# Optimization experiments

Hardware: AMD Instinct MI355X
Metric: run time of the kernel (lower is better)

Reference implementation:

```python
import jax, jax.numpy as jnp
import numpy as np

H = 4      # num_heads
DH = 32    # head dim (hidden_size // num_heads)


def _seg_softmax(logits, seg, n):
    # numerically stable segment softmax over axis 0, segments of size n
    m = jax.ops.segment_max(logits, seg, num_segments=n)
    e = jnp.exp(logits - m[seg])
    s = jax.ops.segment_sum(e, seg, num_segments=n)
    return e / (s[seg] + 1e-16)


def setup_inputs() -> dict:
    key = jax.random.key(0)
    ks = jax.random.split(key, 16)
    N, E, EE, C = 50000, 400000, 800000, 800000
    NIN, EIN, HID, EMB = 1, 32, 128, 32
    inp = {
        'x': jax.random.normal(ks[0], (N, NIN), jnp.float32),
        'edge_index': jax.random.randint(ks[1], (2, E), 0, N),
        'edge_attr': jax.random.normal(ks[2], (E, EIN), jnp.float32),
        'edge_to_edge_index': jax.random.randint(ks[3], (2, EE), 0, E),
        'node_to_node_index': jax.random.randint(ks[4], (2, C), 0, N),
        'W1': jax.random.normal(ks[5], (2 * NIN + EIN, EMB), jnp.float32) / np.sqrt(2 * NIN + EIN),
        'b1': jnp.zeros((EMB,), jnp.float32),
        'W2': jax.random.normal(ks[6], (EMB, HID), jnp.float32) / np.sqrt(EMB),
        'b2': jnp.zeros((HID,), jnp.float32),
        'Wq': jax.random.normal(ks[7], (HID, HID), jnp.float32) / np.sqrt(HID),
        'Wk': jax.random.normal(ks[8], (HID, HID), jnp.float32) / np.sqrt(HID),
        'Wv': jax.random.normal(ks[9], (HID, HID), jnp.float32) / np.sqrt(HID),
        'Wq2': jax.random.normal(ks[10], (1, HID), jnp.float32),
        'Wk2': jax.random.normal(ks[11], (1, HID), jnp.float32),
        'Wv2': jax.random.normal(ks[12], (1, HID), jnp.float32),
    }
    return inp


def reference(x, edge_index, edge_attr, edge_to_edge_index, node_to_node_index,
              W1, b1, W2, b2, Wq, Wk, Wv, Wq2, Wk2, Wv2):
    N = x.shape[0]
    E = edge_attr.shape[0]
    # --- NodeToEdgeAggregation: gather endpoint node feats, concat edge attr, MLP ---
    s, d = edge_index[0], edge_index[1]
    h = jnp.concatenate([x[s], x[d], edge_attr], axis=-1)          # [E, 2*nin+ein]
    h = jax.nn.relu(h @ W1 + b1) @ W2 + b2                          # [E, hidden]
    # --- EdgeToEdgeAggregation: multi-head attention on the line graph ---
    es, ed = edge_to_edge_index[0], edge_to_edge_index[1]
    q = (h @ Wq)[ed].reshape(-1, H, DH)                             # [EE, H, DH]
    k = (h @ Wk)[es].reshape(-1, H, DH)
    v = (h @ Wv)[es].reshape(-1, H, DH)
    logits = (q * k).sum(-1) / jnp.sqrt(jnp.float32(DH))            # [EE, H]
    alpha = _seg_softmax(logits, ed, E)                             # softmax over incoming edge-neighbors
    agg_e = jax.ops.segment_sum(alpha[..., None] * v, ed, num_segments=E)  # [E, H, DH]
    updated_edge_feat = agg_e.reshape(E, -1).mean(axis=1, keepdims=True)   # [E, 1]
    # --- EdgeToNodeAggregation over combined node+edge feature array ---
    nef = jnp.concatenate([x, updated_edge_feat], axis=0)           # [N+E, 1]
    ns, nd = node_to_node_index[0], node_to_node_index[1]
    q2 = (nef[nd] @ Wq2).reshape(-1, H, DH)                         # [C, H, DH]
    k2 = (nef[ns] @ Wk2).reshape(-1, H, DH)
    v2 = (nef[ns] @ Wv2).reshape(-1, H, DH)
    logits2 = (q2 * k2).sum(-1) / jnp.sqrt(jnp.float32(DH))         # [C, H]
    alpha2 = _seg_softmax(logits2, nd, N + E)
    msgs = (alpha2[..., None] * v2).reshape(ns.shape[0], -1).mean(axis=1)  # [C]
    aggregated_node_feat = jax.ops.segment_sum(msgs, nd, num_segments=N)   # [N]
    return (aggregated_node_feat, updated_edge_feat)
```

## Files before the change

kernel.cpp:

```cpp
#include <hip/hip_runtime.h>
#include <stdint.h>

#define HIDN 128
#define EMBN 32
#define PCAP 16
#define NCAP 64
#define PSEGSH 9
#define NSEGSH 7
#define PSEG (1 << PSEGSH)
#define NSEG (1 << NSEGSH)
#define PBCAP 1408
#define NBCAP 2816
#define CHUNK 2048
#define MAXBINS 800

typedef __attribute__((ext_vector_type(8))) short bf16x8;
typedef __attribute__((ext_vector_type(4))) float f32x4;
typedef unsigned long long u64;

__device__ __forceinline__ unsigned bf16r(float f) {
  unsigned u = __float_as_uint(f);
  return (u + 0x7FFFu + ((u >> 16) & 1u)) >> 16;
}
__device__ __forceinline__ unsigned pack2(float a, float b) {
  return bf16r(a) | (bf16r(b) << 16);
}
__device__ __forceinline__ float blo(unsigned u) { return __uint_as_float(u << 16); }
__device__ __forceinline__ float bhi(unsigned u) { return __uint_as_float(u & 0xFFFF0000u); }
__device__ __forceinline__ float4 f4fma(float s, float4 a, float4 b) {
  return make_float4(fmaf(s, a.x, b.x), fmaf(s, a.y, b.y), fmaf(s, a.z, b.z), fmaf(s, a.w, b.w));
}
__device__ __forceinline__ float4 f4max0(float4 a) {
  return make_float4(fmaxf(a.x, 0.f), fmaxf(a.y, 0.f), fmaxf(a.z, 0.f), fmaxf(a.w, 0.f));
}

__global__ __launch_bounds__(256) void k_prep1(
    const float* __restrict__ W2, const float* __restrict__ b2,
    const float* __restrict__ Wq, const float* __restrict__ Wk, const float* __restrict__ Wv,
    float* __restrict__ Wqp, float* __restrict__ Wkp, float* __restrict__ bqp,
    float* __restrict__ Wvsp, float* __restrict__ bvs)
{
  __shared__ float swvs[HIDN * 4];
  int t = threadIdx.x;
  if (blockIdx.x == 33) {
    for (int idx = t; idx < HIDN * 4; idx += 256) {
      int l = idx >> 2, h = idx & 3;
      float s = 0.f;
      const float* wl = Wv + l * HIDN + h * 32;
      for (int dh = 0; dh < 32; dh++) s += wl[dh];
      swvs[idx] = s;
    }
    __syncthreads();
    if (t < 128) {
      int i = t >> 2, h = t & 3;
      float a = 0.f;
      for (int l = 0; l < HIDN; l++) a = fmaf(W2[i * HIDN + l], swvs[l * 4 + h], a);
      Wvsp[t] = a;
    } else if (t < 132) {
      int h = t - 128;
      float a = 0.f;
      for (int l = 0; l < HIDN; l++) a = fmaf(b2[l], swvs[l * 4 + h], a);
      bvs[h] = a;
    }
    return;
  }
  int idx = blockIdx.x * 256 + t;
  if (idx < 8192) {
    int q = idx < 4096;
    int tt = q ? idx : idx - 4096;
    int i = tt >> 7, j = tt & 127;
    const float* W = q ? Wq : Wk;
    float a = 0.f;
    for (int l = 0; l < HIDN; l++)
      a = fmaf(W2[i * HIDN + l], W[l * HIDN + j], a);
    (q ? Wqp : Wkp)[tt] = a;
  } else if (idx < 8320) {
    int j = idx - 8192;
    float a = 0.f;
    for (int l = 0; l < HIDN; l++)
      a = fmaf(b2[l], Wq[l * HIDN + j], a);
    bqp[j] = a;
  }
}

__global__ __launch_bounds__(256, 8) void k_front(
    const float* __restrict__ x, const int* __restrict__ eidx, const float* __restrict__ ea,
    const float* __restrict__ W1, const float* __restrict__ b1,
    const float* __restrict__ Wvsp, const float* __restrict__ bvs,
    unsigned* __restrict__ embB, uint2* __restrict__ vsb,
    const int* __restrict__ e2e, int* __restrict__ goffP, u64* __restrict__ partP,
    const int* __restrict__ n2n, int* __restrict__ goffN, u64* __restrict__ partN,
    const float* __restrict__ Wqp, const float* __restrict__ Wkp, const float* __restrict__ bqp,
    const float* __restrict__ Wq2, const float* __restrict__ Wk2, const float* __restrict__ Wv2,
    unsigned short* __restrict__ MBpk, float* __restrict__ c2th,
    float* __restrict__ dhd, float* __restrict__ wv2s,
    int E, int EE, int C, int N, int nEdgeB, int nPartP, int nPartN, int PBINS, int NBINS)
{
  __shared__ int lcnt[MAXBINS];
  __shared__ int lbase[MAXBINS];
  int b = blockIdx.x;
  int tid = threadIdx.x;
  if (b < nEdgeB) {
    int e = b * 256 + tid;
    if (e >= E) return;
    int si = eidx[e], di = eidx[E + e];
    float xs = x[si], xd = x[di];

    const float4* b4  = (const float4*)b1;
    const float4* w0  = (const float4*)W1;
    const float4* w1r = (const float4*)(W1 + 32);
    float4 E0, E1, E2, E3, E4, E5, E6, E7;
#define INIT(i) E##i = f4fma(xs, w0[i], f4fma(xd, w1r[i], b4[i]));
    INIT(0) INIT(1) INIT(2) INIT(3) INIT(4) INIT(5) INIT(6) INIT(7)
#undef INIT
    const float4* ea4 = (const float4*)(ea + (size_t)e * 32);
#define ROW(c, wr) { const float4* w_ = (const float4*)(W1 + (size_t)(wr) * 32); \
  E0 = f4fma(c, w_[0], E0); E1 = f4fma(c, w_[1], E1); E2 = f4fma(c, w_[2], E2); E3 = f4fma(c, w_[3], E3); \
  E4 = f4fma(c, w_[4], E4); E5 = f4fma(c, w_[5], E5); E6 = f4fma(c, w_[6], E6); E7 = f4fma(c, w_[7], E7); }
#pragma unroll
    for (int rb = 0; rb < 8; rb++) {
      float4 v = ea4[rb];
      ROW(v.x, 2 + rb * 4 + 0)
      ROW(v.y, 2 + rb * 4 + 1)
      ROW(v.z, 2 + rb * 4 + 2)
      ROW(v.w, 2 + rb * 4 + 3)
    }
#undef ROW
    E0 = f4max0(E0); E1 = f4max0(E1); E2 = f4max0(E2); E3 = f4max0(E3);
    E4 = f4max0(E4); E5 = f4max0(E5); E6 = f4max0(E6); E7 = f4max0(E7);

    uint4 p0, p1, p2, p3;
    p0.x = pack2(E0.x, E0.y); p0.y = pack2(E0.z, E0.w); p0.z = pack2(E1.x, E1.y); p0.w = pack2(E1.z, E1.w);
    p1.x = pack2(E2.x, E2.y); p1.y = pack2(E2.z, E2.w); p1.z = pack2(E3.x, E3.y); p1.w = pack2(E3.z, E3.w);
    p2.x = pack2(E4.x, E4.y); p2.y = pack2(E4.z, E4.w); p2.z = pack2(E5.x, E5.y); p2.w = pack2(E5.z, E5.w);
    p3.x = pack2(E6.x, E6.y); p3.y = pack2(E6.z, E6.w); p3.z = pack2(E7.x, E7.y); p3.w = pack2(E7.z, E7.w);
    uint4* er = (uint4*)(embB + (size_t)e * 16);
    er[0] = p0; er[1] = p1; er[2] = p2; er[3] = p3;

    const float4* wv = (const float4*)Wvsp;
    float4 vs = *(const float4*)bvs;
#define VK(k) { vs = f4fma(E##k.x, wv[4*k+0], vs); vs = f4fma(E##k.y, wv[4*k+1], vs); \
                vs = f4fma(E##k.z, wv[4*k+2], vs); vs = f4fma(E##k.w, wv[4*k+3], vs); }
    VK(0) VK(1) VK(2) VK(3) VK(4) VK(5) VK(6) VK(7)
#undef VK
    vsb[e] = make_uint2(pack2(vs.x, vs.y), pack2(vs.z, vs.w));
  } else if (b < nEdgeB + nPartP) {
    int start = (b - nEdgeB) * CHUNK;
    for (int i = tid; i < PBINS; i += 256) lcnt[i] = 0;
    __syncthreads();
#pragma unroll 4
    for (int k = 0; k < 8; k++) {
      int p = start + k * 256 + tid;
      if (p < EE) atomicAdd(&lcnt[e2e[EE + p] >> PSEGSH], 1);
    }
    __syncthreads();
    for (int i = tid; i < PBINS; i += 256) {
      int c = lcnt[i];
      lbase[i] = c ? atomicAdd(&goffP[i], c) : 0;
      lcnt[i] = 0;
    }
    __syncthreads();
#pragma unroll 4
    for (int k = 0; k < 8; k++) {
      int p = start + k * 256 + tid;
      if (p < EE) {
        int es = e2e[p], ed = e2e[EE + p];
        int bin = ed >> PSEGSH;
        int pos = atomicAdd(&lcnt[bin], 1) + lbase[bin];
        if (pos < PBCAP)
          partP[(size_t)bin * PBCAP + pos] = ((u64)(unsigned)ed << 32) | (unsigned)es;
      }
    }
  } else if (b < nEdgeB + nPartP + nPartN) {
    int start = (b - nEdgeB - nPartP) * CHUNK;
    for (int i = tid; i < NBINS; i += 256) lcnt[i] = 0;
    __syncthreads();
#pragma unroll 4
    for (int k = 0; k < 8; k++) {
      int c = start + k * 256 + tid;
      if (c < C) {
        int nd = n2n[C + c];
        if (nd < N) atomicAdd(&lcnt[nd >> NSEGSH], 1);
      }
    }
    __syncthreads();
    for (int i = tid; i < NBINS; i += 256) {
      int c = lcnt[i];
      lbase[i] = c ? atomicAdd(&goffN[i], c) : 0;
      lcnt[i] = 0;
    }
    __syncthreads();
#pragma unroll 4
    for (int k = 0; k < 8; k++) {
      int c = start + k * 256 + tid;
      if (c < C) {
        int ns = n2n[c], nd = n2n[C + c];
        if (nd < N) {
          int bin = nd >> NSEGSH;
          unsigned pay = __float_as_uint(x[ns]);
          int pos = atomicAdd(&lcnt[bin], 1) + lbase[bin];
          if (pos < NBCAP)
            partN[(size_t)bin * NBCAP + pos] = ((u64)(unsigned)nd << 32) | pay;
        }
      }
    }
  } else {
    const float rs = 0.17677669529663687f;
    int idx = (b - nEdgeB - nPartP - nPartN) * 256 + tid;
    if (idx < 4096) {
      int jj = idx & 7, lane = (idx >> 3) & 63, nb = (idx >> 9) & 1, h = idx >> 10;
      int k = (lane >> 4) * 8 + jj;
      int n = nb * 16 + (lane & 15);
      float a = 0.f;
      const float* wq = Wqp + k * HIDN + h * 32;
      const float* wk = Wkp + n * HIDN + h * 32;
      for (int j = 0; j < 32; j++) a = fmaf(wq[j], wk[j], a);
      MBpk[idx] = (unsigned short)bf16r(a * rs);
    } else if (idx < 4224) {
      int t = idx - 4096;
      int h = t >> 5, ip = t & 31;
      float a2 = 0.f;
      for (int j = 0; j < 32; j++)
        a2 = fmaf(bqp[h * 32 + j], Wkp[ip * HIDN + h * 32 + j], a2);
      c2th[h * 32 + ip] = a2 * rs;
    } else if (idx < 4228) {
      int h = idx - 4224;
      float d = 0.f, wsum = 0.f;
      for (int dh = 0; dh < 32; dh++) {
        d = fmaf(Wq2[h * 32 + dh], Wk2[h * 32 + dh], d);
        wsum += Wv2[h * 32 + dh];
      }
      dhd[h]  = d * rs;
      wv2s[h] = wsum;
    }
  }
}

__global__ __launch_bounds__(256, 4) void k_fill(
    const int* __restrict__ goffP, const u64* __restrict__ partP,
    int* __restrict__ pcnt, int* __restrict__ pbucket,
    int E)
{
  extern __shared__ int lds[];
  int b = blockIdx.x;
  int tid = threadIdx.x;
  int seg0 = b << PSEGSH;
  int nseg = E - seg0; if (nseg > PSEG) nseg = PSEG;
  int* cnt = lds;
  int* rows = lds + PSEG;
  for (int i = tid; i < nseg; i += 256) cnt[i] = 0;
  __syncthreads();
  int g = goffP[b]; if (g > PBCAP) g = PBCAP;
  for (int i = tid; i < g; i += 256) {
    u64 pk = partP[(size_t)b * PBCAP + i];
    int ed = (int)(pk >> 32);
    int es = (int)(unsigned)pk;
    int s = ed - seg0;
    int pos = atomicAdd(&cnt[s], 1);
    if (pos < PCAP) rows[s * PCAP + pos] = es;
  }
  __syncthreads();
  for (int i = tid; i < nseg; i += 256) pcnt[seg0 + i] = cnt[i];
  int tot = nseg * PCAP;
  for (int i = tid; i < tot; i += 256)
    pbucket[(size_t)seg0 * PCAP + i] = rows[i];
}

__global__ __launch_bounds__(256, 4) void k_back(
    const unsigned* __restrict__ embB, const unsigned short* __restrict__ MBpk,
    const uint2* __restrict__ vsb, const float* __restrict__ c2th,
    const int* __restrict__ pcnt, const int* __restrict__ pbucket,
    const int* __restrict__ goffN, const u64* __restrict__ partN,
    const float* __restrict__ x, const float* __restrict__ dhd, const float* __restrict__ wv2s,
    float* __restrict__ out0, float* __restrict__ out1,
    int E, int N, int NBINS)
{
  __shared__ float qtl[256 * 33];
  int b = blockIdx.x;
  int tid = threadIdx.x;
  if (b < NBINS) {
    int seg0 = b << NSEGSH;
    int nseg = N - seg0; if (nseg > NSEG) nseg = NSEG;
    int* cnt = (int*)qtl;
    float* rows = qtl + NSEG;
    for (int i = tid; i < nseg; i += 256) cnt[i] = 0;
    __syncthreads();
    int g = goffN[b]; if (g > NBCAP) g = NBCAP;
    for (int i = tid; i < g; i += 256) {
      u64 pk = partN[(size_t)b * NBCAP + i];
      int nd = (int)(pk >> 32);
      int s = nd - seg0;
      int pos = atomicAdd(&cnt[s], 1);
      if (pos < NCAP) rows[s * (NCAP + 1) + pos] = __uint_as_float((unsigned)pk);
    }
    __syncthreads();
    for (int t = tid; t < nseg * 4; t += 256) {
      int s = t >> 2, h = t & 3;
      int c = cnt[s]; c = c < NCAP ? c : NCAP;
      int nd = seg0 + s;
      float xn = x[nd];
      float d = dhd[h];
      const float* bkt = rows + s * (NCAP + 1);

      float amx = -3.4e38f, amn = 3.4e38f;
      for (int n = 0; n < c; n++) {
        float a = xn * bkt[n];
        amx = fmaxf(amx, a); amn = fminf(amn, a);
      }
      float m = (d > 0.f) ? d * amx : d * amn;

      float den = 0.f, num = 0.f;
      for (int n = 0; n < c; n++) {
        float asv = bkt[n];
        float ev = __expf(fmaf(xn * asv, d, -m));
        den += ev;
        num = fmaf(ev, asv, num);
      }
      float r = wv2s[h] * num / (den + 1e-16f);
      r += __shfl_xor(r, 1);
      r += __shfl_xor(r, 2);
      if (h == 0) out0[nd] = r * 0.0078125f;
    }
  } else {
    int pb = b - NBINS;
    int wave = tid >> 6, lane = tid & 63;
    int e0 = pb * 64;
    int we0 = e0 + wave * 16;

    int e = e0 + (tid >> 2);
    int h = tid & 3;
    int eL = (e < E) ? e : (E - 1);
    int cnt = pcnt[eL];
    uint4 r0 = *(const uint4*)(pbucket + ((size_t)eL << 4));

    union { uint4 u; bf16x8 bv; } af;
    af.u = *((const uint4*)(embB + ((size_t)(we0 + (lane & 15)) << 4)) + (lane >> 4));

#pragma unroll
    for (int hh = 0; hh < 4; hh++) {
#pragma unroll
      for (int nb = 0; nb < 2; nb++) {
        union { uint4 u; bf16x8 bv; } bf;
        bf.u = *(const uint4*)(MBpk + (((hh * 2 + nb) * 64 + lane) << 3));
        int col = nb * 16 + (lane & 15);
        float c2v = c2th[hh * 32 + col];
        f32x4 acc = {c2v, c2v, c2v, c2v};
        acc = __builtin_amdgcn_mfma_f32_16x16x32_bf16(af.bv, bf.bv, acc, 0, 0, 0);
        int rowb = wave * 16 + (lane >> 4) * 4;
#pragma unroll
        for (int r = 0; r < 4; r++)
          qtl[((rowb + r) * 4 + hh) * 33 + col] = acc[r];
      }
    }

    cnt = cnt < PCAP ? cnt : PCAP;
    int s0 = (cnt > 0) ? r0.x : 0;
    int s1 = (cnt > 1) ? r0.y : 0;
    int s2 = (cnt > 2) ? r0.z : 0;
    int s3 = (cnt > 3) ? r0.w : 0;
#define GATH(i) \
    const uint4* ep##i = (const uint4*)(embB + ((size_t)s##i << 4)); \
    uint4 u##i##0 = ep##i[0], u##i##1 = ep##i[1], u##i##2 = ep##i[2], u##i##3 = ep##i[3]; \
    uint2 vu##i = vsb[s##i];
    GATH(0) GATH(1) GATH(2) GATH(3)
#undef GATH

    __syncthreads();

    if (e >= E) return;
    const float* q = qtl + tid * 33;

    float den = 0.f, num = 0.f;
#define DOT8(uu, base) \
      dot = fmaf(q[base + 0], blo(uu.x), dot); dot = fmaf(q[base + 1], bhi(uu.x), dot); \
      dot = fmaf(q[base + 2], blo(uu.y), dot); dot = fmaf(q[base + 3], bhi(uu.y), dot); \
      dot = fmaf(q[base + 4], blo(uu.z), dot); dot = fmaf(q[base + 5], bhi(uu.z), dot); \
      dot = fmaf(q[base + 6], blo(uu.w), dot); dot = fmaf(q[base + 7], bhi(uu.w), dot);
#define SLOT(i) { \
      float dot = 0.f; \
      DOT8(u##i##0, 0) DOT8(u##i##1, 8) DOT8(u##i##2, 16) DOT8(u##i##3, 24) \
      unsigned vh = (h & 2) ? vu##i.y : vu##i.x; \
      float vsv = (h & 1) ? bhi(vh) : blo(vh); \
      float ex = (i < cnt) ? __expf(dot) : 0.f; \
      den += ex; \
      num = fmaf(ex, vsv, num); }
    SLOT(0) SLOT(1) SLOT(2) SLOT(3)
#undef SLOT

    for (int n = 4; n < cnt; n++) {
      int es = pbucket[((size_t)e << 4) + n];
      const uint4* ep = (const uint4*)(embB + ((size_t)es << 4));
      uint4 t0 = ep[0], t1 = ep[1], t2 = ep[2], t3 = ep[3];
      uint2 vu = vsb[es];
      unsigned vh = (h & 2) ? vu.y : vu.x;
      float vsv = (h & 1) ? bhi(vh) : blo(vh);
      float dot = 0.f;
      DOT8(t0, 0) DOT8(t1, 8) DOT8(t2, 16) DOT8(t3, 24)
      float ex = __expf(dot);
      den += ex;
      num = fmaf(ex, vsv, num);
    }
#undef DOT8

    float r = num / (den + 1e-16f);
    r += __shfl_xor(r, 1);
    r += __shfl_xor(r, 2);
    if (h == 0) out1[e] = r * 0.0078125f;
  }
}

extern "C" void kernel_launch(void* const* d_in, const int* in_sizes, int n_in,
                              void* d_out, int out_size, void* d_ws, size_t ws_size,
                              hipStream_t stream)
{
  const float* x   = (const float*)d_in[0];
  const int*   eidx= (const int*)d_in[1];
  const float* ea  = (const float*)d_in[2];
  const int*   e2e = (const int*)d_in[3];
  const int*   n2n = (const int*)d_in[4];
  const float* W1  = (const float*)d_in[5];
  const float* b1  = (const float*)d_in[6];
  const float* W2  = (const float*)d_in[7];
  const float* b2  = (const float*)d_in[8];
  const float* Wq  = (const float*)d_in[9];
  const float* Wk  = (const float*)d_in[10];
  const float* Wv  = (const float*)d_in[11];
  const float* Wq2 = (const float*)d_in[12];
  const float* Wk2 = (const float*)d_in[13];
  const float* Wv2 = (const float*)d_in[14];

  const int N  = in_sizes[0];
  const int E  = in_sizes[1] / 2;
  const int EE = in_sizes[3] / 2;
  const int C  = in_sizes[4] / 2;

  float* out0 = (float*)d_out;
  float* out1 = (float*)d_out + N;

  const int PBINS = (E + PSEG - 1) >> PSEGSH;
  const int NBINS = (N + NSEG - 1) >> NSEGSH;

  char* w = (char*)d_ws;
  size_t off = 0;
  auto alloc = [&](size_t bytes) -> char* {
    char* p = w + off;
    off += (bytes + 255) & ~(size_t)255;
    return p;
  };
  float* Wqp   = (float*)alloc(EMBN * HIDN * 4);
  float* Wkp   = (float*)alloc(EMBN * HIDN * 4);
  float* bqp   = (float*)alloc(HIDN * 4);
  unsigned short* MBpk = (unsigned short*)alloc(4096 * 2);
  float* c2th  = (float*)alloc(4 * EMBN * 4);
  float* Wvsp  = (float*)alloc(EMBN * 4 * 4);
  float* bvs   = (float*)alloc(16);
  float* dhd   = (float*)alloc(16);
  float* wv2s  = (float*)alloc(16);
  unsigned* embB = (unsigned*)alloc((size_t)E * 16 * 4);
  uint2* vsb   = (uint2*)alloc((size_t)E * 8);
  u64*   partP = (u64*)alloc((size_t)PBINS * PBCAP * 8);
  u64*   partN = (u64*)alloc((size_t)NBINS * NBCAP * 8);
  int*   pbucket = (int*)alloc((size_t)E * PCAP * 4);
  int*   pcnt  = (int*)alloc((size_t)E * 4);
  char* zbase = w + off;
  int*   goffP = (int*)alloc((size_t)PBINS * 4);
  int*   goffN = (int*)alloc((size_t)NBINS * 4);
  size_t zbytes = (size_t)((w + off) - zbase);

  const int nEdgeB = (E + 255) / 256;
  const int nPartP = (EE + CHUNK - 1) / CHUNK;
  const int nPartN = (C + CHUNK - 1) / CHUNK;
  const int nPairMfmaB = (E + 63) / 64;
  const int nPrep2B = 17;
  const size_t fillLDS = (size_t)(PSEG + PSEG * PCAP) * 4;

  hipMemsetAsync(zbase, 0, zbytes, stream);

  k_prep1<<<34, 256, 0, stream>>>(W2, b2, Wq, Wk, Wv, Wqp, Wkp, bqp, Wvsp, bvs);
  k_front<<<nEdgeB + nPartP + nPartN + nPrep2B, 256, 0, stream>>>(
      x, eidx, ea, W1, b1, Wvsp, bvs, embB, vsb,
      e2e, goffP, partP, n2n, goffN, partN,
      Wqp, Wkp, bqp, Wq2, Wk2, Wv2, MBpk, c2th, dhd, wv2s,
      E, EE, C, N, nEdgeB, nPartP, nPartN, PBINS, NBINS);
  k_fill<<<PBINS, 256, fillLDS, stream>>>(goffP, partP, pcnt, pbucket, E);
  k_back<<<NBINS + nPairMfmaB, 256, 0, stream>>>(
      embB, MBpk, vsb, c2th, pcnt, pbucket, goffN, partN,
      x, dhd, wv2s, out0, out1, E, N, NBINS);
}
```

Measured before the change: 245.1 us.

## Fuse edge-pair bucket fill into k_back via per-block LDS binning

Removes the k_fill kernel and the global pbucket/pcnt arrays. Each 64-edge block in k_back now scans its whole 1024-edge partition bin from partP and keeps only the pairs that land in its own 64 edges, building the neighbor lists in LDS. Bin size and capacity are doubled to match. This drops one launch and a global write/read round trip. In exchange each partition bin is read redundantly by 16 blocks, and the block adds LDS usage and an extra barrier.

After: 241.9 us. No clear change (-1.3%).

```diff
diff --git a/kernel.cpp b/kernel.cpp
--- a/kernel.cpp
+++ b/kernel.cpp
@@ -5,14 +5,14 @@
 #define EMBN 32
 #define PCAP 16
 #define NCAP 64
-#define PSEGSH 9
+#define PSEGSH 10
 #define NSEGSH 7
 #define PSEG (1 << PSEGSH)
 #define NSEG (1 << NSEGSH)
-#define PBCAP 1408
+#define PBCAP 2816
 #define NBCAP 2816
 #define CHUNK 2048
-#define MAXBINS 800
+#define MAXBINS 400
 
 typedef __attribute__((ext_vector_type(8))) short bf16x8;
 typedef __attribute__((ext_vector_type(4))) float f32x4;
@@ -236,46 +236,18 @@
   }
 }
 
-__global__ __launch_bounds__(256, 4) void k_fill(
-    const int* __restrict__ goffP, const u64* __restrict__ partP,
-    int* __restrict__ pcnt, int* __restrict__ pbucket,
-    int E)
-{
-  extern __shared__ int lds[];
-  int b = blockIdx.x;
-  int tid = threadIdx.x;
-  int seg0 = b << PSEGSH;
-  int nseg = E - seg0; if (nseg > PSEG) nseg = PSEG;
-  int* cnt = lds;
-  int* rows = lds + PSEG;
-  for (int i = tid; i < nseg; i += 256) cnt[i] = 0;
-  __syncthreads();
-  int g = goffP[b]; if (g > PBCAP) g = PBCAP;
-  for (int i = tid; i < g; i += 256) {
-    u64 pk = partP[(size_t)b * PBCAP + i];
-    int ed = (int)(pk >> 32);
-    int es = (int)(unsigned)pk;
-    int s = ed - seg0;
-    int pos = atomicAdd(&cnt[s], 1);
-    if (pos < PCAP) rows[s * PCAP + pos] = es;
-  }
-  __syncthreads();
-  for (int i = tid; i < nseg; i += 256) pcnt[seg0 + i] = cnt[i];
-  int tot = nseg * PCAP;
-  for (int i = tid; i < tot; i += 256)
-    pbucket[(size_t)seg0 * PCAP + i] = rows[i];
-}
-
 __global__ __launch_bounds__(256, 4) void k_back(
     const unsigned* __restrict__ embB, const unsigned short* __restrict__ MBpk,
     const uint2* __restrict__ vsb, const float* __restrict__ c2th,
-    const int* __restrict__ pcnt, const int* __restrict__ pbucket,
+    const int* __restrict__ goffP, const u64* __restrict__ partP,
     const int* __restrict__ goffN, const u64* __restrict__ partN,
     const float* __restrict__ x, const float* __restrict__ dhd, const float* __restrict__ wv2s,
     float* __restrict__ out0, float* __restrict__ out1,
     int E, int N, int NBINS)
 {
   __shared__ float qtl[256 * 33];
+  __shared__ int pcntL[64];
+  __shared__ int prows[64 * 17];
   int b = blockIdx.x;
   int tid = threadIdx.x;
   if (b < NBINS) {
@@ -325,16 +297,27 @@
     int pb = b - NBINS;
     int wave = tid >> 6, lane = tid & 63;
     int e0 = pb * 64;
+    int bin = e0 >> PSEGSH;
     int we0 = e0 + wave * 16;
 
-    int e = e0 + (tid >> 2);
-    int h = tid & 3;
-    int eL = (e < E) ? e : (E - 1);
-    int cnt = pcnt[eL];
-    uint4 r0 = *(const uint4*)(pbucket + ((size_t)eL << 4));
+    if (tid < 64) pcntL[tid] = 0;
 
     union { uint4 u; bf16x8 bv; } af;
     af.u = *((const uint4*)(embB + ((size_t)(we0 + (lane & 15)) << 4)) + (lane >> 4));
+
+    __syncthreads();
+
+    int g = goffP[bin]; if (g > PBCAP) g = PBCAP;
+    const u64* binp = partP + (size_t)bin * PBCAP;
+    for (int i = tid; i < g; i += 256) {
+      u64 pk = binp[i];
+      int ed = (int)(pk >> 32);
+      unsigned s = (unsigned)(ed - e0);
+      if (s < 64u) {
+        int pos = atomicAdd(&pcntL[s], 1);
+        if (pos < PCAP) prows[s * 17 + pos] = (int)(unsigned)pk;
+      }
+    }
 
 #pragma unroll
     for (int hh = 0; hh < 4; hh++) {
@@ -353,22 +336,28 @@
       }
     }
 
+    __syncthreads();
+
+    int e = e0 + (tid >> 2);
+    if (e >= E) return;
+    int h = tid & 3;
+    const float* q = qtl + tid * 33;
+    int sloc = tid >> 2;
+    const int* rowp = prows + sloc * 17;
+
+    int cnt = pcntL[sloc];
     cnt = cnt < PCAP ? cnt : PCAP;
-    int s0 = (cnt > 0) ? r0.x : 0;
-    int s1 = (cnt > 1) ? r0.y : 0;
-    int s2 = (cnt > 2) ? r0.z : 0;
-    int s3 = (cnt > 3) ? r0.w : 0;
+
+    int s0 = (cnt > 0) ? rowp[0] : 0;
+    int s1 = (cnt > 1) ? rowp[1] : 0;
+    int s2 = (cnt > 2) ? rowp[2] : 0;
+    int s3 = (cnt > 3) ? rowp[3] : 0;
 #define GATH(i) \
     const uint4* ep##i = (const uint4*)(embB + ((size_t)s##i << 4)); \
     uint4 u##i##0 = ep##i[0], u##i##1 = ep##i[1], u##i##2 = ep##i[2], u##i##3 = ep##i[3]; \
     uint2 vu##i = vsb[s##i];
     GATH(0) GATH(1) GATH(2) GATH(3)
 #undef GATH
-
-    __syncthreads();
-
-    if (e >= E) return;
-    const float* q = qtl + tid * 33;
 
     float den = 0.f, num = 0.f;
 #define DOT8(uu, base) \
@@ -388,7 +377,7 @@
 #undef SLOT
 
     for (int n = 4; n < cnt; n++) {
-      int es = pbucket[((size_t)e << 4) + n];
+      int es = rowp[n];
       const uint4* ep = (const uint4*)(embB + ((size_t)es << 4));
       uint4 t0 = ep[0], t1 = ep[1], t2 = ep[2], t3 = ep[3];
       uint2 vu = vsb[es];
@@ -460,8 +449,6 @@
   uint2* vsb   = (uint2*)alloc((size_t)E * 8);
   u64*   partP = (u64*)alloc((size_t)PBINS * PBCAP * 8);
   u64*   partN = (u64*)alloc((size_t)NBINS * NBCAP * 8);
-  int*   pbucket = (int*)alloc((size_t)E * PCAP * 4);
-  int*   pcnt  = (int*)alloc((size_t)E * 4);
   char* zbase = w + off;
   int*   goffP = (int*)alloc((size_t)PBINS * 4);
   int*   goffN = (int*)alloc((size_t)NBINS * 4);
@@ -472,7 +459,6 @@
   const int nPartN = (C + CHUNK - 1) / CHUNK;
   const int nPairMfmaB = (E + 63) / 64;
   const int nPrep2B = 17;
-  const size_t fillLDS = (size_t)(PSEG + PSEG * PCAP) * 4;
 
   hipMemsetAsync(zbase, 0, zbytes, stream);
 
@@ -482,8 +468,7 @@
       e2e, goffP, partP, n2n, goffN, partN,
       Wqp, Wkp, bqp, Wq2, Wk2, Wv2, MBpk, c2th, dhd, wv2s,
       E, EE, C, N, nEdgeB, nPartP, nPartN, PBINS, NBINS);
-  k_fill<<<PBINS, 256, fillLDS, stream>>>(goffP, partP, pcnt, pbucket, E);
   k_back<<<NBINS + nPairMfmaB, 256, 0, stream>>>(
-      embB, MBpk, vsb, c2th, pcnt, pbucket, goffN, partN,
+      embB, MBpk, vsb, c2th, goffP, partP, goffN, partN,
       x, dhd, wv2s, out0, out1, E, N, NBINS);
 }
```
